# Performance work log

Hardware: AMD Instinct MI355X
Metric: run time of the kernel (lower is better)

The kernel has to match this reference:

```python
import jax, jax.numpy as jnp
import numpy as np

B, H, W = 1, 64, 64
Q = 256 * 256
CIN, ENC, HID, HEADS = 3, 64, 256, 16
HC = HID // HEADS
IN0 = (2 + HID) * 4 + 2   # 1034
IN1 = 2 + HID + 2         # 260


def conv3x3(x, w, b):
    y = jax.lax.conv_general_dilated(x, w, (1, 1), ((1, 1), (1, 1)),
                                     dimension_numbers=("NCHW", "OIHW", "NCHW"))
    return y + b[None, :, None, None]


def gelu(x):
    return jax.nn.gelu(x, approximate=False)


def mlp(x, w1, b1, w2, b2):
    # dropout p=0.0 -> identity
    return gelu(x @ w1 + b1) @ w2 + b2


def custom_ln(x, w, b, eps=1e-5):
    # torch .std() uses Bessel correction (ddof=1); note (std + eps), not var
    mean = x.mean(-1, keepdims=True)
    std = jnp.std(x, axis=-1, ddof=1, keepdims=True)
    return w * ((x - mean) / (std + eps)) + b


def qkv_attn(x, qkv_w, qkv_b, kln_w, kln_b, vln_w, vln_b, proj_w, proj_b):
    Bn, HWn, C = x.shape
    bias = x
    qkv = (x @ qkv_w + qkv_b).reshape(Bn, HWn, HEADS, 3 * HC).transpose(0, 2, 1, 3)
    q, k, v = jnp.split(qkv, 3, axis=-1)          # each [B, heads, HW, hc]
    k = custom_ln(k, kln_w, kln_b)
    v = custom_ln(v, vln_w, vln_b)
    kv = jnp.einsum("bhnc,bhnd->bhcd", k, v) / HWn  # linear attention: O(HW)
    v = jnp.einsum("bhnc,bhcd->bhnd", q, kv)
    v = v.transpose(0, 2, 1, 3).reshape(Bn, HWn, C)
    ret = v + bias
    return gelu(ret @ proj_w + proj_b) + bias


def _unnorm(c, size):  # align_corners=False
    return ((c + 1.0) * size - 1.0) / 2.0


def gs_nearest(img, coord_yx):
    # img [B,C,H,W]; coord_yx [B,Q,2] in (-1,1), (y,x) order (torch grid is flipped)
    Bn, C, Hn, Wn = img.shape
    iy = jnp.clip(jnp.round(_unnorm(coord_yx[..., 0], Hn)).astype(jnp.int32), 0, Hn - 1)
    ix = jnp.clip(jnp.round(_unnorm(coord_yx[..., 1], Wn)).astype(jnp.int32), 0, Wn - 1)
    flat = img.reshape(Bn, C, Hn * Wn)
    out = jnp.take_along_axis(flat, (iy * Wn + ix)[:, None, :], axis=2)  # [B,C,Q]
    return out.transpose(0, 2, 1)


def gs_bilinear(img, coord_yx, border=False):
    Bn, C, Hn, Wn = img.shape
    fy = _unnorm(coord_yx[..., 0], Hn)
    fx = _unnorm(coord_yx[..., 1], Wn)
    if border:
        fy = jnp.clip(fy, 0.0, Hn - 1.0)
        fx = jnp.clip(fx, 0.0, Wn - 1.0)
    y0 = jnp.floor(fy)
    x0 = jnp.floor(fx)
    wy = (fy - y0)[:, None, :]
    wx = (fx - x0)[:, None, :]
    y0i = y0.astype(jnp.int32)
    x0i = x0.astype(jnp.int32)
    flat = img.reshape(Bn, C, Hn * Wn)

    def gather(yi, xi):
        ok = (yi >= 0) & (yi < Hn) & (xi >= 0) & (xi < Wn)
        yc = jnp.clip(yi, 0, Hn - 1)
        xc = jnp.clip(xi, 0, Wn - 1)
        g = jnp.take_along_axis(flat, (yc * Wn + xc)[:, None, :], axis=2)
        return g * ok[:, None, :].astype(img.dtype)

    v00 = gather(y0i, x0i)
    v01 = gather(y0i, x0i + 1)
    v10 = gather(y0i + 1, x0i)
    v11 = gather(y0i + 1, x0i + 1)
    out = (v00 * (1 - wy) * (1 - wx) + v01 * (1 - wy) * wx +
           v10 * wy * (1 - wx) + v11 * wy * wx)
    return out.transpose(0, 2, 1)


def _forward(inp, coord, cell,
             enc_w, enc_b, freq_w, freq_b,
             out0_w1, out0_b1, out0_w2, out0_b2,
             out1_w1, out1_b1, out1_w2, out1_b2,
             a0_qkv_w, a0_qkv_b, a0_kln_w, a0_kln_b, a0_vln_w, a0_vln_b, a0_proj_w, a0_proj_b,
             a1_qkv_w, a1_qkv_b, a1_kln_w, a1_kln_b, a1_vln_w, a1_vln_b, a1_proj_w, a1_proj_b,
             fc1_w1, fc1_b1, fc1_w2, fc1_b2,
             fc2_w1, fc2_b1, fc2_w2, fc2_b2):
    Bq, Qn = coord.shape[:2]
    feat = conv3x3(inp, enc_w, enc_b)        # encoder stub [B,ENC,H,W]
    freq = conv3x3(feat, freq_w, freq_b)     # [B,HID,H,W]
    Hn, Wn = feat.shape[-2], feat.shape[-1]
    # make_coord(H,W): pixel-centered coords in (-1,1); channel0=y, channel1=x
    ys = -1.0 + (2.0 * jnp.arange(Hn, dtype=jnp.float32) + 1.0) / Hn
    xs = -1.0 + (2.0 * jnp.arange(Wn, dtype=jnp.float32) + 1.0) / Wn
    fc = jnp.stack(jnp.meshgrid(ys, xs, indexing="ij"), axis=0)  # [2,H,W]
    feat_coord = jnp.broadcast_to(fc[None], (Bq, 2, Hn, Wn))
    rx, ry = 1.0 / Hn, 1.0 / Wn               # 2/H/2, 2/W/2
    eps = 1e-6
    offs = jnp.array([[vx * rx + eps, vy * ry + eps]
                      for vx in (-1, 1) for vy in (-1, 1)], jnp.float32)  # [4,2]
    coord_s = jnp.clip(coord[None] + offs[:, None, None, :], -1 + 1e-6, 1 - 1e-6)  # [4,B,Q,2]
    q_freq = jax.vmap(gs_nearest, in_axes=(None, 0))(freq, coord_s)        # [4,B,Q,HID]
    q_coord = jax.vmap(gs_nearest, in_axes=(None, 0))(feat_coord, coord_s)  # [4,B,Q,2]
    scale = jnp.array([Hn, Wn], jnp.float32)
    rel = (coord[None] - q_coord) * scale                                  # [4,B,Q,2]
    areas = jnp.abs(rel[..., 0] * rel[..., 1]) + 1e-9                      # [4,B,Q]
    tot = areas.sum(0)
    areas_sw = areas[::-1]  # swap(0,3), swap(1,2)
    preds = q_freq * (areas_sw / tot)[..., None]
    rel_cell = cell * scale
    grid0 = jnp.concatenate([
        jnp.moveaxis(rel, 0, 2).reshape(Bq, Qn, 8),
        jnp.moveaxis(preds, 0, 2).reshape(Bq, Qn, 4 * HID),
        rel_cell], axis=-1)                                                # [B,Q,1034]
    grid_pred = gs_bilinear(freq, coord)                                   # [B,Q,HID]
    grid1 = jnp.concatenate([coord, grid_pred, rel_cell], axis=-1)         # [B,Q,260]
    x0 = qkv_attn(mlp(grid0, out0_w1, out0_b1, out0_w2, out0_b2),
                  a0_qkv_w, a0_qkv_b, a0_kln_w, a0_kln_b, a0_vln_w, a0_vln_b, a0_proj_w, a0_proj_b)
    x1 = qkv_attn(mlp(grid1, out1_w1, out1_b1, out1_w2, out1_b2),
                  a1_qkv_w, a1_qkv_b, a1_kln_w, a1_kln_b, a1_vln_w, a1_vln_b, a1_proj_w, a1_proj_b)
    f = x0 + x1
    result = mlp(f + gelu(mlp(f, fc1_w1, fc1_b1, fc1_w2, fc1_b2)),
                 fc2_w1, fc2_b1, fc2_w2, fc2_b2)                           # [B,Q,3]
    result_bil = gs_bilinear(inp, coord, border=True)                      # [B,Q,3]
    return result + result_bil


def setup_inputs() -> dict:
    key = jax.random.key(0)
    ks = iter(jax.random.split(key, 64))

    def n(shape, s=0.02):
        return jax.random.normal(next(ks), shape, jnp.float32) * s

    inp = jax.random.normal(next(ks), (B, CIN, H, W), jnp.float32)
    coord = jax.random.uniform(next(ks), (B, Q, 2), jnp.float32, -1.0, 1.0)
    cell = jnp.full((B, Q, 2), 2.0 / 256.0, jnp.float32)
    d = dict(inp=inp, coord=coord, cell=cell,
             enc_w=n((ENC, CIN, 3, 3)), enc_b=jnp.zeros((ENC,), jnp.float32),
             freq_w=n((HID, ENC, 3, 3)), freq_b=jnp.zeros((HID,), jnp.float32),
             out0_w1=n((IN0, HID)), out0_b1=jnp.zeros((HID,), jnp.float32),
             out0_w2=n((HID, HID)), out0_b2=jnp.zeros((HID,), jnp.float32),
             out1_w1=n((IN1, HID)), out1_b1=jnp.zeros((HID,), jnp.float32),
             out1_w2=n((HID, HID)), out1_b2=jnp.zeros((HID,), jnp.float32),
             fc1_w1=n((HID, HID)), fc1_b1=jnp.zeros((HID,), jnp.float32),
             fc1_w2=n((HID, HID)), fc1_b2=jnp.zeros((HID,), jnp.float32),
             fc2_w1=n((HID, HID)), fc2_b1=jnp.zeros((HID,), jnp.float32),
             fc2_w2=n((HID, 3)), fc2_b2=jnp.zeros((3,), jnp.float32))
    for p in ("a0", "a1"):
        d[p + "_qkv_w"] = n((HID, 3 * HID))
        d[p + "_qkv_b"] = jnp.zeros((3 * HID,), jnp.float32)
        d[p + "_kln_w"] = jnp.ones((HEADS, 1, HC), jnp.float32)
        d[p + "_kln_b"] = jnp.zeros((HEADS, 1, HC), jnp.float32)
        d[p + "_vln_w"] = jnp.ones((HEADS, 1, HC), jnp.float32)
        d[p + "_vln_b"] = jnp.zeros((HEADS, 1, HC), jnp.float32)
        d[p + "_proj_w"] = n((HID, HID))
        d[p + "_proj_b"] = jnp.zeros((HID,), jnp.float32)
    return d


def reference(inp, coord, cell,
              enc_w, enc_b, freq_w, freq_b,
              out0_w1, out0_b1, out0_w2, out0_b2,
              out1_w1, out1_b1, out1_w2, out1_b2,
              a0_qkv_w, a0_qkv_b, a0_kln_w, a0_kln_b, a0_vln_w, a0_vln_b, a0_proj_w, a0_proj_b,
              a1_qkv_w, a1_qkv_b, a1_kln_w, a1_kln_b, a1_vln_w, a1_vln_b, a1_proj_w, a1_proj_b,
              fc1_w1, fc1_b1, fc1_w2, fc1_b2,
              fc2_w1, fc2_b1, fc2_w2, fc2_b2):
    return _forward(inp, coord, cell,
                    enc_w, enc_b, freq_w, freq_b,
                    out0_w1, out0_b1, out0_w2, out0_b2,
                    out1_w1, out1_b1, out1_w2, out1_b2,
                    a0_qkv_w, a0_qkv_b, a0_kln_w, a0_kln_b, a0_vln_w, a0_vln_b, a0_proj_w, a0_proj_b,
                    a1_qkv_w, a1_qkv_b, a1_kln_w, a1_kln_b, a1_vln_w, a1_vln_b, a1_proj_w, a1_proj_b,
                    fc1_w1, fc1_b1, fc1_w2, fc1_b2,
                    fc2_w1, fc2_b1, fc2_w2, fc2_b2)
```

## Files before the change

### kernel.cpp

```cpp
#include <hip/hip_runtime.h>
#include <hip/hip_bf16.h>

#define DI __device__ __forceinline__

DI float gelu_f(float x){ return 0.5f*x*(1.0f + erff(x*0.7071067811865476f)); }
DI float bf2f(__hip_bfloat16 b){ return __bfloat162float(b); }
DI __hip_bfloat16 f2bf(float f){ return __float2bfloat16(f); }
DI float bflo(unsigned u){ return __uint_as_float(u<<16); }
DI float bfhi(unsigned u){ return __uint_as_float(u & 0xffff0000u); }
DI unsigned pack2bf(float a, float b){
  __hip_bfloat16 ha = f2bf(a), hb = f2bf(b);
  unsigned short ua = *reinterpret_cast<unsigned short*>(&ha);
  unsigned short ub = *reinterpret_cast<unsigned short*>(&hb);
  return (unsigned)ua | ((unsigned)ub<<16);
}

typedef __attribute__((ext_vector_type(8))) short bf16x8;
typedef __attribute__((ext_vector_type(4))) float f32x4;

template<typename T>
DI void load_lds16(const T* g, T* l){
  __builtin_amdgcn_global_load_lds((const __attribute__((address_space(1))) void*)g,
                                   (__attribute__((address_space(3))) void*)l, 16, 0, 0);
}
// ... 40 lines not shown
  int j = blockIdx.x, kk = threadIdx.x;
  float v;
  if(j < 1024){
    int s = j>>8, n = j&255;
    v = w0[(8 + 256*s + kk)*256 + n];
  } else {
    v = w1[(2 + kk)*256 + (j-1024)];
  }
  wt[(size_t)j*256 + kk] = f2bf(v);
}

struct PrepDesc { const float* src; __hip_bfloat16* dst; int mode; int pad; };
struct PrepArgs { PrepDesc d[13]; };
__global__ __launch_bounds__(256) void k_prep(PrepArgs a){
  int u = blockIdx.x >> 8, b = blockIdx.x & 255, t = threadIdx.x;
  PrepDesc d = a.d[u];
  float v;
  if(d.mode == 0) v = d.src[t*256 + b];
  else { int col = 48*(b>>4) + (d.mode-1) + (b&15); v = d.src[t*768 + col]; }
  d.dst[b*256 + t] = f2bf(v);
}

__global__ __launch_bounds__(256) void k_biasperm(const float* __restrict__ b0, const float* __restrict__ b1,
    const float* kw0, const float* kb0, const float* vw0, const float* vb0,
    const float* kw1, const float* kb1, const float* vw1, const float* vb1,
    float* __restrict__ dstB, float* __restrict__ lnw2, float* __restrict__ lnb2,
    __hip_bfloat16* __restrict__ zpage){
  int t = threadIdx.x;
  zpage[t] = f2bf(0.0f);
  #pragma unroll
  for(int br=0;br<2;br++){
    const float* s = br ? b1 : b0;
    #pragma unroll
    for(int part=0;part<3;part++)
      dstB[br*768 + part*256 + t] = s[48*(t>>4) + part*16 + (t&15)];
  }
  #pragma unroll
  for(int br=0;br<2;br++){
    #pragma unroll
    for(int half=0;half<2;half++){
      int j = half*256 + t;
      int h = j>>5, idx = j&31;
      bool isK = idx<16;
      int c = isK ? idx : idx-16;
      const float* w = isK ? (br?kw1:kw0) : (br?vw1:vw0);
      const float* bb= isK ? (br?kb1:kb0) : (br?vb1:vb0);
      lnw2[br*512 + j] = w[h*16+c];
      lnb2[br*512 + j] = bb[h*16+c];
    }
  }
}

template<int ADDI>
__global__ __launch_bounds__(256) void k_smallmm(const __hip_bfloat16* __restrict__ A,
    const __hip_bfloat16* __restrict__ B, __hip_bfloat16* __restrict__ C){
  __shared__ float ar[256];
  int i = blockIdx.x, t = threadIdx.x;
  float a = bf2f(A[(size_t)i*256 + t]);
  if(ADDI && t==i) a += 1.0f;
  ar[t] = a;
  __syncthreads();
  float a0=0.f,a1=0.f,a2=0.f,a3=0.f;
  for(int l=0;l<256;l+=4){
    a0 += ar[l+0]*bf2f(B[(l+0)*256 + t]);
    a1 += ar[l+1]*bf2f(B[(l+1)*256 + t]);
    a2 += ar[l+2]*bf2f(B[(l+2)*256 + t]);
    a3 += ar[l+3]*bf2f(B[(l+3)*256 + t]);
  }
  C[(size_t)i*256 + t] = f2bf((a0+a1)+(a2+a3));
}

__global__ __launch_bounds__(256) void k_smallmmR(const __hip_bfloat16* __restrict__ A,
    const __hip_bfloat16* __restrict__ B, __hip_bfloat16* __restrict__ C){
  __shared__ float ar[256];
  int j = blockIdx.x, t = threadIdx.x;
  int src = kvmap(j);
  ar[t] = bf2f(A[(size_t)src*256 + t]);
  __syncthreads();
  float a0=0.f,a1=0.f,a2=0.f,a3=0.f;
  for(int l=0;l<256;l+=4){
    a0 += ar[l+0]*bf2f(B[(l+0)*256 + t]);
    a1 += ar[l+1]*bf2f(B[(l+1)*256 + t]);
    a2 += ar[l+2]*bf2f(B[(l+2)*256 + t]);
    a3 += ar[l+3]*bf2f(B[(l+3)*256 + t]);
  }
  C[(size_t)j*256 + t] = f2bf((a0+a1)+(a2+a3));
}

__global__ __launch_bounds__(256) void k_bkv2R(const float* __restrict__ b2, const float* __restrict__ biaskv,
    const __hip_bfloat16* __restrict__ kvT_, float* __restrict__ outb){
  __shared__ float s_b2[256];
  int t = threadIdx.x; int n = blockIdx.x*256 + t;
  int src = kvmap(n);
  s_b2[t] = b2[t];
  __syncthreads();
  float v = biaskv[src];
  for(int l=0;l<256;l++) v += s_b2[l]*bf2f(kvT_[(size_t)src*256 + l]);
  outb[n] = v;
}

__global__ __launch_bounds__(256) void k_cvec(const float* __restrict__ b2, const float* __restrict__ bfold,
    const __hip_bfloat16* __restrict__ WfoldT, const __hip_bfloat16* __restrict__ projT_,
    const float* __restrict__ bp, float* __restrict__ c1){
  __shared__ float s_b2[256], s_r[256];
  int t = threadIdx.x;
  s_b2[t] = b2[t];
  __syncthreads();
  float r = s_b2[t] + bfold[t];
  for(int l=0;l<256;l++) r += s_b2[l]*bf2f(WfoldT[(size_t)t*256 + l]);
  s_r[t] = r;
  __syncthreads();
  float c = bp[t];
  for(int l=0;l<256;l++) c += s_r[l]*bf2f(projT_[(size_t)t*256 + l]);
  c1[t] = c;
}

__global__ __launch_bounds__(256) void k_sample(const float* __restrict__ coord, const float* __restrict__ inp,
    float* __restrict__ mf, int* __restrict__ mi, float* __restrict__ bil){
  int q = blockIdx.x*256 + threadIdx.x;
  float cy = coord[2*q], cx = coord[2*q+1];
  const float LO = (float)(-1.0 + 1e-6), HI = (float)(1.0 - 1e-6);
  const float ONEG = (float)(-1.0/64.0 + 1e-6), OPOS = (float)(1.0/64.0 + 1e-6);
  float areas[4];
  #pragma unroll
  for(int s=0;s<4;s++){
    float oy = (s<2)?ONEG:OPOS;
    float ox = (s&1)?OPOS:ONEG;
    float csy = fminf(fmaxf(cy+oy, LO), HI);
    float csx = fminf(fmaxf(cx+ox, LO), HI);
    float fy = ((csy+1.0f)*64.0f - 1.0f)*0.5f;
    float fx = ((csx+1.0f)*64.0f - 1.0f)*0.5f;
    int iy = (int)rintf(fy); iy = iy<0?0:(iy>63?63:iy);
    int ix = (int)rintf(fx); ix = ix<0?0:(ix>63?63:ix);
    float qcy = -1.0f + (float)(2*iy+1)*0.015625f;
    float qcx = -1.0f + (float)(2*ix+1)*0.015625f;
    float ry = (cy-qcy)*64.0f, rx = (cx-qcx)*64.0f;
    mf[q*16 + 4 + 2*s] = ry; mf[q*16 + 5 + 2*s] = rx;
    areas[s] = fabsf(ry*rx) + 1e-9f;
    mi[q*8 + s] = iy*64 + ix;
  }
  float tot = areas[0]+areas[1]+areas[2]+areas[3];
  #pragma unroll
  for(int s=0;s<4;s++) mf[q*16 + s] = areas[3-s] / tot;

  float fy = ((cy+1.0f)*64.0f - 1.0f)*0.5f;
  float fx = ((cx+1.0f)*64.0f - 1.0f)*0.5f;
  {
    float y0 = floorf(fy), x0 = floorf(fx);
    float wy = fy-y0, wx = fx-x0;
    int y0i = (int)y0, x0i = (int)x0;
    float cw[4] = {(1.0f-wy)*(1.0f-wx), (1.0f-wy)*wx, wy*(1.0f-wx), wy*wx};
    #pragma unroll
    for(int c2=0;c2<4;c2++){
      int yi = y0i + (c2>>1), xi = x0i + (c2&1);
      bool ok = (yi>=0 && yi<64 && xi>=0 && xi<64);
      int yc = yi<0?0:(yi>63?63:yi), xc = xi<0?0:(xi>63?63:xi);
      mf[q*16 + 12 + c2] = ok ? cw[c2] : 0.0f;
      mi[q*8 + 4 + c2] = yc*64 + xc;
    }
  }
  {
    float fyb = fminf(fmaxf(fy, 0.0f), 63.0f);
    float fxb = fminf(fmaxf(fx, 0.0f), 63.0f);
    float y0 = floorf(fyb), x0 = floorf(fxb);
    float wy = fyb-y0, wx = fxb-x0;
    int y0i = (int)y0, x0i = (int)x0;
    float cw[4] = {(1.0f-wy)*(1.0f-wx), (1.0f-wy)*wx, wy*(1.0f-wx), wy*wx};
    float a0=0,a1=0,a2=0;
    #pragma unroll
    for(int c2=0;c2<4;c2++){
      int yi = y0i + (c2>>1), xi = x0i + (c2&1);
      if(yi>=0 && yi<64 && xi>=0 && xi<64){
        int idx = yi*64+xi; float wgt = cw[c2];
        a0 += inp[idx]*wgt; a1 += inp[4096+idx]*wgt; a2 += inp[8192+idx]*wgt;
      }
    }
    bil[q*3+0]=a0; bil[q*3+1]=a1; bil[q*3+2]=a2;
  }
}

template<int BR>
__global__ __launch_bounds__(256) void k_stage1(const __hip_bfloat16* __restrict__ P, const float* __restrict__ mf,
    const int* __restrict__ mi, const float* __restrict__ coord, const float* __restrict__ cell,
    const float* __restrict__ W1, const float* __restrict__ b1, __hip_bfloat16* __restrict__ out){
  __shared__ float wsm[11][256];
  int j = threadIdx.x;
  if(BR==0){
    #pragma unroll
    for(int r=0;r<8;r++) wsm[r][j] = W1[r*256 + j];
    wsm[8][j] = W1[1032*256 + j];
    wsm[9][j] = W1[1033*256 + j];
    wsm[10][j] = b1[j];
  } else {
    wsm[0][j] = W1[0*256 + j];
    wsm[1][j] = W1[1*256 + j];
    wsm[2][j] = W1[258*256 + j];
    wsm[3][j] = W1[259*256 + j];
    wsm[4][j] = b1[j];
  }
  __syncthreads();
  int q0 = blockIdx.x*32;
  for(int qq=0;qq<32;qq++){
    int q = q0+qq;
    float acc;
    const float* m = mf + q*16;
    const int* ii = mi + q*8;
    if(BR==0){
      acc = wsm[10][j];
      #pragma unroll
      for(int r=0;r<8;r++) acc += m[4+r]*wsm[r][j];
      float cly = cell[2*q]*64.0f, clx = cell[2*q+1]*64.0f;
      acc += cly*wsm[8][j] + clx*wsm[9][j];
      #pragma unroll
      for(int s=0;s<4;s++) acc += m[s]*bf2f(P[(size_t)ii[s]*1280 + s*256 + j]);
    } else {
      acc = wsm[4][j];
      float cy = coord[2*q], cx = coord[2*q+1];
      float cly = cell[2*q]*64.0f, clx = cell[2*q+1]*64.0f;
      acc += cy*wsm[0][j] + cx*wsm[1][j] + cly*wsm[2][j] + clx*wsm[3][j];
      #pragma unroll
      for(int c2=0;c2<4;c2++) acc += m[12+c2]*bf2f(P[(size_t)ii[4+c2]*1280 + 1024 + j]);
    }
    out[(size_t)q*256 + j] = f2bf(gelu_f(acc));
  }
}

template<int ACT,int NRES>
__global__ __launch_bounds__(512) void k_gemm_mfma(
    const __hip_bfloat16* __restrict__ A, const __hip_bfloat16* __restrict__ BT,
    const float* __restrict__ bias, const __hip_bfloat16* __restrict__ R1,
    const __hip_bfloat16* __restrict__ R2, __hip_bfloat16* __restrict__ C,
    int M, int N, int K, int ldc){
  __shared__ __align__(1024) char smem[64*133*4];
  const int t = threadIdx.x, wave = t>>6, lane = t&63;
  const int MT = M>>7, NT = N>>7;
  const int b = blockIdx.x, xcd = b&7, i = b>>3;
  const int nt = i % NT, mtl = i / NT;
  const int m0 = (xcd*(MT>>3) + mtl) << 7, n0 = nt << 7;
  const int wr = (wave>>2)*64, wc = (wave&3)*32;
  const int lr = lane&15, lh = lane>>4;

  f32x4 acc[4][2] = {};
  const int ntiles = K>>6;
  for(int kt=0; kt<ntiles; ++kt){
    __syncthreads();
    #pragma unroll
    for(int q2=0;q2<2;q2++){
      int c = (wave*2+q2)*64 + lane;
      int row = c>>3; int k8 = (c&7) ^ (row&7);
      __hip_bfloat16* la = (__hip_bfloat16*)smem + (size_t)(wave*2+q2)*512;
      __hip_bfloat16* lb = (__hip_bfloat16*)(smem + 16384) + (size_t)(wave*2+q2)*512;
      load_lds16(A  + (size_t)(m0+row)*K + (kt*64 + k8*8), la);
      load_lds16(BT + (size_t)(n0+row)*K + (kt*64 + k8*8), lb);
    }
    __syncthreads();
    const __hip_bfloat16* Ab = (const __hip_bfloat16*)smem;
    const __hip_bfloat16* Bb = (const __hip_bfloat16*)(smem + 16384);
    #pragma unroll
    for(int kk=0;kk<2;kk++){
      bf16x8 af[4], bfr[2];
// ... 113 lines not shown
        int p = (kk*4 + lh) ^ (row&7);
        af[m] = *reinterpret_cast<const bf16x8*>(Ab + row*64 + p*8);
      }
      #pragma unroll
      for(int n=0;n<4;n++){
        int row = wc + n*16 + lr;
        int p = (kk*4 + lh) ^ (row&7);
        bfr[n] = *reinterpret_cast<const bf16x8*>(Bb + row*64 + p*8);
      }
      #pragma unroll
      for(int m=0;m<4;m++)
        #pragma unroll
        for(int n=0;n<4;n++)
          acc[m][n] = __builtin_amdgcn_mfma_f32_16x16x32_bf16(af[m], bfr[n], acc[m][n], 0,0,0);
    }
  }

  float* epi = (float*)smem;
  const int cg = t&3;
  #pragma unroll
  for(int hf=0; hf<2; ++hf){
    __syncthreads();
    if((wave>>1) == hf){
      #pragma unroll
      for(int m=0;m<4;m++)
        #pragma unroll
        for(int n=0;n<4;n++){
          int col = wc + n*16 + lr;
          #pragma unroll
          for(int j=0;j<4;j++)
            epi[(m*16 + lh*4 + j)*133 + col] = acc[m][n][j];
        }
    }
    __syncthreads();
    const int lrow = t>>2, c0 = cg*32;
    const size_t grow = (size_t)(m0 + hf*64 + lrow);
    const float* er = epi + lrow*133;
    #pragma unroll
    for(int g0=0; g0<4; g0++){
      int g = (g0 + cg) & 3;
      int cb = c0 + g*8;
      int gc = n0 + cb;
      float v[8];
      #pragma unroll
      for(int e=0;e<8;e++) v[e] = er[cb+e] + bias[gc+e];
      uint4 o;
      o.x = pack2bf(v[0],v[1]); o.y = pack2bf(v[2],v[3]);
      o.z = pack2bf(v[4],v[5]); o.w = pack2bf(v[6],v[7]);
      *reinterpret_cast<uint4*>(C + grow*256 + gc) = o;
    }
  }
}

__global__ __launch_bounds__(512) void k_kvln(
    const __hip_bfloat16* __restrict__ A, const __hip_bfloat16* __restrict__ BT,
    const float* __restrict__ bias, const float* __restrict__ lnw, const float* __restrict__ lnb,
    float* __restrict__ kvpart){
  __shared__ __align__(1024) char smem[34816];
  const int t = threadIdx.x, wave = t>>6, lane = t&63;
  const int MT = 512, NT = 4;
  const int b = blockIdx.x, xcd = b&7, i = b>>3;
  const int nt = i % NT, mtl = i / NT;
  const int m0 = (xcd*(MT>>3) + mtl) << 7, n0 = nt << 7;
  const int wr = (wave>>2)*64, wc = (wave&3)*32;
  const int lr = lane&15, lh = lane>>4;

  f32x4 acc[4][2] = {};
  for(int kt=0; kt<4; ++kt){
    __syncthreads();
    #pragma unroll
    for(int q2=0;q2<2;q2++){
      int c = (wave*2+q2)*64 + lane;
      int row = c>>3; int k8 = (c&7) ^ (row&7);
      __hip_bfloat16* la = (__hip_bfloat16*)smem + (size_t)(wave*2+q2)*512;
      __hip_bfloat16* lb = (__hip_bfloat16*)(smem + 16384) + (size_t)(wave*2+q2)*512;
      load_lds16(A  + (size_t)(m0+row)*256 + (kt*64 + k8*8), la);
      load_lds16(BT + (size_t)(n0+row)*256 + (kt*64 + k8*8), lb);
    }
    __syncthreads();
    const __hip_bfloat16* Ab = (const __hip_bfloat16*)smem;
    const __hip_bfloat16* Bb = (const __hip_bfloat16*)(smem + 16384);
    #pragma unroll
    for(int kk=0;kk<2;kk++){
      bf16x8 af[4], bfr[2];
      #pragma unroll
      for(int m=0;m<4;m++){
        int row = wr + m*16 + lr;
        int p = (kk*4 + lh) ^ (row&7);
        af[m] = *reinterpret_cast<const bf16x8*>(Ab + row*64 + p*8);
      }
      #pragma unroll
      for(int n=0;n<2;n++){
        int row = wc + n*16 + lr;
        int p = (kk*4 + lh) ^ (row&7);
        bfr[n] = *reinterpret_cast<const bf16x8*>(Bb + row*64 + p*8);
      }
      #pragma unroll
      for(int m=0;m<4;m++)
        #pragma unroll
        for(int n=0;n<2;n++)
          acc[m][n] = __builtin_amdgcn_mfma_f32_16x16x32_bf16(af[m], bfr[n], acc[m][n], 0,0,0);
    }
  }
  __syncthreads();

  __hip_bfloat16* knT = (__hip_bfloat16*)smem;
  __hip_bfloat16* vnT = (__hip_bfloat16*)(smem + 17408);
  #pragma unroll
  for(int m=0;m<4;m++){
    #pragma unroll
    for(int n=0;n<2;n++){
      int cl = wc + n*16 + lr;
      int gcol = n0 + cl;
      float bs = bias[gcol];
      int h2 = cl>>5, isV = (cl>>4)&1;
      short4 pk;
      #pragma unroll
      for(int j=0;j<4;j++) ((__hip_bfloat16*)&pk)[j] = f2bf(acc[m][n][j] + bs);
      int r = wr + m*16 + lh*4;
      __hip_bfloat16* dst = (isV ? vnT : knT) + (h2*16 + lr)*136 + r;
      *reinterpret_cast<short4*>(dst) = pk;
    }
  }
  __syncthreads();
  #pragma unroll
  for(int i4=0; i4<2; ++i4){
    int task = i4*512 + t;
    int r = task & 127, hv = task >> 7;
    int h2 = hv >> 1, isV = hv & 1;
    __hip_bfloat16* base = (isV ? vnT : knT) + (h2*16)*136 + r;
    float xs[16];
    float s=0.0f, s2=0.0f;
    #pragma unroll
    for(int c=0;c<16;c++){ xs[c] = bf2f(base[c*136]); s += xs[c]; s2 += xs[c]*xs[c]; }
    float mean = s*0.0625f;
    float var = (s2 - 16.0f*mean*mean)*(1.0f/15.0f); var = var<0.0f?0.0f:var;
    float inv = 1.0f/(sqrtf(var) + 1e-5f);
    int gbase = n0 + h2*32 + isV*16;
    #pragma unroll
    for(int c=0;c<16;c++)
      base[c*136] = f2bf(lnw[gbase+c]*((xs[c]-mean)*inv) + lnb[gbase+c]);
  }
  __syncthreads();
  {
    const int hloc = wave>>1, kh = wave&1;
    f32x4 kacc = {};
    #pragma unroll
    for(int kk=0;kk<2;kk++){
      int off = kh*64 + kk*32 + lh*8;
      bf16x8 af  = *reinterpret_cast<const bf16x8*>(knT + (hloc*16 + lr)*136 + off);
      bf16x8 bf_ = *reinterpret_cast<const bf16x8*>(vnT + (hloc*16 + lr)*136 + off);
      kacc = __builtin_amdgcn_mfma_f32_16x16x32_bf16(af, bf_, kacc, 0,0,0);
    }
    const int mt = m0>>7;
    const int hglob = nt*4 + hloc;
    #pragma unroll
    for(int j=0;j<4;j++)
      kvpart[((size_t)mt*2 + kh)*4096 + hglob*256 + (lh*4+j)*16 + lr] = kacc[j];
  }
}

template<int NRES>
__global__ __launch_bounds__(512) void k_gemm12(
    const __hip_bfloat16* __restrict__ A, const __hip_bfloat16* __restrict__ B1T,
    const float* __restrict__ c1, const __hip_bfloat16* __restrict__ B2T,
    const float* __restrict__ b2, const __hip_bfloat16* __restrict__ R,
    __hip_bfloat16* __restrict__ C){
  __shared__ __align__(1024) char smem[49152];
  const int t = threadIdx.x, wave = t>>6, lane = t&63;
  const int MT = 512, NT = 2;
  const int b = blockIdx.x, xcd = b&7, i = b>>3;
  const int nt = i % NT, mtl = i / NT;
  const int m0 = (xcd*(MT>>3) + mtl) << 7, n0 = nt << 7;
  const int wr = (wave>>2)*64, wc = (wave&3)*32;
  const int lr = lane&15, lh = lane>>4;
  f32x4 acc1[4][2] = {}, acc2[4][2] = {};
  for(int k0=0;k0<256;k0+=64){
    __syncthreads();
    #pragma unroll
    for(int q2=0;q2<2;q2++){
      int c = (wave*2+q2)*64 + lane;
      int row = c>>3; int k8 = (c&7) ^ (row&7);
      __hip_bfloat16* base = (__hip_bfloat16*)smem + (size_t)(wave*2+q2)*512;
      load_lds16(A   + (size_t)(m0+row)*256 + (k0 + k8*8), base);
      load_lds16(B1T + (size_t)(n0+row)*256 + (k0 + k8*8), base + 8192);
      load_lds16(B2T + (size_t)(n0+row)*256 + (k0 + k8*8), base + 16384);
    }
    __syncthreads();
    const __hip_bfloat16* Ab = (const __hip_bfloat16*)smem;
    #pragma unroll
    for(int kk=0;kk<2;kk++){
      bf16x8 af[4], bfr[2];
      #pragma unroll
      for(int m=0;m<4;m++){
        int row = wr + m*16 + lr;
        int p = (kk*4 + lh) ^ (row&7);
        af[m] = *reinterpret_cast<const bf16x8*>(Ab + row*64 + p*8);
      }
      #pragma unroll
      for(int n=0;n<2;n++){
        int row = wc + n*16 + lr;
        int p = (kk*4 + lh) ^ (row&7);
        bfr[n] = *reinterpret_cast<const bf16x8*>(Ab + 8192 + row*64 + p*8);
      }
      #pragma unroll
      for(int m=0;m<4;m++)
        #pragma unroll
        for(int n=0;n<2;n++)
          acc1[m][n] = __builtin_amdgcn_mfma_f32_16x16x32_bf16(af[m], bfr[n], acc1[m][n], 0,0,0);
      #pragma unroll
      for(int n=0;n<2;n++){
// ... 118 lines not shown
      for(int m=0;m<4;m++)
        #pragma unroll
        for(int n=0;n<2;n++)
          acc[m][n] = __builtin_amdgcn_mfma_f32_16x16x32_bf16(af[m], bfr[n], acc[m][n], 0,0,0);
    }
  }

  float* epi = (float*)smem;
  #pragma unroll
  for(int hf=0; hf<2; ++hf){
    __syncthreads();
    if((wave>>2) == hf){
      #pragma unroll
      for(int m=0;m<4;m++)
        #pragma unroll
        for(int n=0;n<2;n++){
          int col = wc + n*16 + lr;
          #pragma unroll
          for(int j=0;j<4;j++)
            epi[(m*16 + lh*4 + j)*133 + col] = acc[m][n][j];
        }
    }
    __syncthreads();
    {
      const int lrow = t>>3, c0 = (t&7)*16;
      const float* er = epi + lrow*133;
      float s0=0.f, s1=0.f, s2=0.f;
      #pragma unroll
      for(int e=0;e<16;e++){
        int gc = n0 + c0 + e;
        float v = gelu_f(er[c0+e] + bias[gc]);
        s0 += v*w4s[gc*3+0];
        s1 += v*w4s[gc*3+1];
        s2 += v*w4s[gc*3+2];
      }
      s0 += __shfl_xor(s0,1); s0 += __shfl_xor(s0,2); s0 += __shfl_xor(s0,4);
      s1 += __shfl_xor(s1,1); s1 += __shfl_xor(s1,2); s1 += __shfl_xor(s1,4);
      s2 += __shfl_xor(s2,1); s2 += __shfl_xor(s2,2); s2 += __shfl_xor(s2,4);
      if((t&7)==0){
        float* pp = part + (size_t)nt*196608 + (size_t)(m0 + hf*64 + lrow)*3;
        pp[0]=s0; pp[1]=s1; pp[2]=s2;
      }
    }
  }
}

__global__ __launch_bounds__(256) void k_combine(const float* __restrict__ part, const float* __restrict__ b4,
    const float* __restrict__ bil, float* __restrict__ out){
  int i = blockIdx.x*256 + threadIdx.x;
  int j = i - (i/3)*3;
  out[i] = part[i] + part[196608 + i] + b4[j] + bil[i];
}

__global__ __launch_bounds__(256) void k_kvred(const float* __restrict__ kvpart, float* __restrict__ kv){
  __shared__ float sm[256];
  int b = blockIdx.x, t = threadIdx.x;
  int d = t & 15, seg = t >> 4;
  float s = 0.0f;
  for(int k=0;k<64;k++) s += kvpart[(size_t)(seg*64+k)*4096 + b*16 + d];
  sm[t] = s;
  __syncthreads();
  if(t < 16){
    float r = 0.0f;
    #pragma unroll
    for(int g=0; g<16; g++) r += sm[g*16 + t];
    kv[b*16 + t] = r * (1.0f/65536.0f);
  }
}

__global__ __launch_bounds__(256) void k_fold(const __hip_bfloat16* __restrict__ qT,
    const float* __restrict__ biasq, const float* __restrict__ kv,
    __hip_bfloat16* __restrict__ WfoldT, float* __restrict__ bfold){
  int n = blockIdx.x, t = threadIdx.x;
  int h = n>>4, d = n&15;
  float s = 0.0f;
  #pragma unroll
  for(int c=0;c<16;c++)
    s += bf2f(qT[(size_t)(h*16+c)*256 + t]) * kv[h*256 + c*16 + d];
  WfoldT[(size_t)n*256 + t] = f2bf(s);
  if(t==0){
    float b=0.0f;
    #pragma unroll
    for(int c=0;c<16;c++) b += biasq[h*16+c]*kv[h*256+c*16+d];
    bfold[n]=b;
  }
}

extern "C" void kernel_launch(void* const* d_in, const int* in_sizes, int n_in,
                              void* d_out, int out_size, void* d_ws, size_t ws_size,
                              hipStream_t stream){
  (void)in_sizes; (void)n_in; (void)out_size;
  const float* inp     = (const float*)d_in[0];
  const float* coord   = (const float*)d_in[1];
  const float* cell    = (const float*)d_in[2];
  const float* enc_w   = (const float*)d_in[3];
  const float* enc_b   = (const float*)d_in[4];
  const float* freq_w  = (const float*)d_in[5];
  const float* freq_b  = (const float*)d_in[6];
  const float* out0_w1 = (const float*)d_in[7];
  const float* out0_b1 = (const float*)d_in[8];
  const float* out0_w2 = (const float*)d_in[9];
  const float* out0_b2 = (const float*)d_in[10];
  const float* out1_w1 = (const float*)d_in[11];
  const float* out1_b1 = (const float*)d_in[12];
  const float* out1_w2 = (const float*)d_in[13];
  const float* out1_b2 = (const float*)d_in[14];
  const float* fc1_w1  = (const float*)d_in[15];
  const float* fc1_b1  = (const float*)d_in[16];
  const float* fc1_w2  = (const float*)d_in[17];
  const float* fc1_b2  = (const float*)d_in[18];
  const float* fc2_w1  = (const float*)d_in[19];
  const float* fc2_b1  = (const float*)d_in[20];
  const float* fc2_w2  = (const float*)d_in[21];
  const float* fc2_b2  = (const float*)d_in[22];
  const float* qkv_w[2] = {(const float*)d_in[23], (const float*)d_in[31]};
  const float* qkv_b[2] = {(const float*)d_in[24], (const float*)d_in[32]};
  const float* kln_w[2] = {(const float*)d_in[25], (const float*)d_in[33]};
  const float* kln_b[2] = {(const float*)d_in[26], (const float*)d_in[34]};
  const float* vln_w[2] = {(const float*)d_in[27], (const float*)d_in[35]};
  const float* vln_b[2] = {(const float*)d_in[28], (const float*)d_in[36]};
  const float* proj_w[2] = {(const float*)d_in[29], (const float*)d_in[37]};
  const float* proj_b[2] = {(const float*)d_in[30], (const float*)d_in[38]};
  const float* b2arr[2] = {out0_b2, out1_b2};

  char* wsp = (char*)d_ws; size_t off = 0;
  auto alloc = [&](size_t bytes)->void*{ void* p = wsp + off; off += (bytes + 255) & ~(size_t)255; return p; };
  __hip_bfloat16* featP = (__hip_bfloat16*)alloc(262144ull*2);
  __hip_bfloat16* zpage = (__hip_bfloat16*)alloc(256ull*2);
  __hip_bfloat16* wtb = (__hip_bfloat16*)alloc(2097152ull*2);
  __hip_bfloat16* P = (__hip_bfloat16*)alloc(5242880ull*2);
  float* mf     = (float*)alloc(65536ull*16*4);
  int*   mi     = (int*)alloc(65536ull*8*4);
  float* bil    = (float*)alloc(65536ull*3*4);
  float* kvpart = (float*)alloc(1024ull*4096*4);
  float* kv0    = (float*)alloc(4096ull*4);
  float* kv1    = (float*)alloc(4096ull*4);
  float* biasbuf= (float*)alloc(1536ull*4);
  float* lnbuf  = (float*)alloc(2048ull*4);
  float* bfold  = (float*)alloc(256ull*4);
  float* c1     = (float*)alloc(256ull*4);
  float* bkvh   = (float*)alloc(1024ull*4);
  float* part   = (float*)alloc(2ull*196608*4);
  __hip_bfloat16* wfoldT = (__hip_bfloat16*)alloc(65536ull*2);
  __hip_bfloat16* bufA = (__hip_bfloat16*)alloc(65536ull*256*2);
  __hip_bfloat16* bufB = (__hip_bfloat16*)alloc(65536ull*256*2);
  __hip_bfloat16* bufC = (__hip_bfloat16*)alloc(65536ull*256*2);
  if(off > ws_size) return;

  __hip_bfloat16* w2T[2]   = {wtb,          wtb + 65536};
  __hip_bfloat16* projT[2] = {wtb + 131072, wtb + 196608};
  __hip_bfloat16* fc1w1T   =  wtb + 262144;
  __hip_bfloat16* fc1w2T   =  wtb + 327680;
  __hip_bfloat16* fc2w1T   =  wtb + 393216;
  __hip_bfloat16* qT[2]    = {wtb + 458752, wtb + 655360};
  __hip_bfloat16* kvT[2]   = {wtb + 524288, wtb + 720896};
  __hip_bfloat16* wfreqT   =  wtb + 851968;
  __hip_bfloat16* wblkT    =  wtb + 1015808;
  __hip_bfloat16* kvh2T[2] = {wtb + 1343488, wtb + 1474560};
  __hip_bfloat16* Ubuf     =  wtb + 1605632;
  __hip_bfloat16* M1T      =  wtb + 1671168;
  __hip_bfloat16* freqB = bufB;

  k_conv1<<<1024,256,0,stream>>>(inp, enc_w, enc_b, featP);
  k_wfreq<<<256,256,0,stream>>>(freq_w, wfreqT);
  k_wblk<<<1280,256,0,stream>>>(out0_w1, out1_w1, wblkT);

  PrepArgs pa;
  pa.d[0]  = {out0_w2,   w2T[0],   0, 0};
  pa.d[1]  = {out1_w2,   w2T[1],   0, 0};
  pa.d[2]  = {proj_w[0], projT[0], 0, 0};
  pa.d[3]  = {proj_w[1], projT[1], 0, 0};
  pa.d[4]  = {fc1_w1,    fc1w1T,   0, 0};
  pa.d[5]  = {fc1_w2,    fc1w2T,   0, 0};
  pa.d[6]  = {fc2_w1,    fc2w1T,   0, 0};
  pa.d[7]  = {qkv_w[0],  qT[0],    1, 0};
  pa.d[8]  = {qkv_w[0],  kvT[0],   17, 0};
  pa.d[9]  = {qkv_w[0],  kvT[0]+65536, 33, 0};
  pa.d[10] = {qkv_w[1],  qT[1],    1, 0};
  pa.d[11] = {qkv_w[1],  kvT[1],   17, 0};
  pa.d[12] = {qkv_w[1],  kvT[1]+65536, 33, 0};
  k_prep<<<13*256,256,0,stream>>>(pa);
  k_biasperm<<<1,256,0,stream>>>(qkv_b[0], qkv_b[1],
      kln_w[0], kln_b[0], vln_w[0], vln_b[0], kln_w[1], kln_b[1], vln_w[1], vln_b[1],
      biasbuf, lnbuf, lnbuf + 1024, zpage);

  for(int br=0;br<2;br++){
    k_smallmmR<<<512,256,0,stream>>>(kvT[br], w2T[br], kvh2T[br]);
    k_bkv2R<<<2,256,0,stream>>>(b2arr[br], biasbuf + br*768 + 256, kvT[br], bkvh + br*512);
  }

  k_gfreq<<<64,256,0,stream>>>(featP, zpage, wfreqT, freq_b, freqB);
  k_gemm_mfma<0,0><<<320,512,0,stream>>>(freqB, wblkT, nullptr, nullptr,nullptr, P, 4096,1280,256, 1280);

  k_sample<<<256,256,0,stream>>>(coord, inp, mf, mi, bil);

  for(int br=0;br<2;br++){
    if(br==0) k_stage1<0><<<2048,256,0,stream>>>(P, mf, mi, coord, cell, out0_w1, out0_b1, bufA);
    else      k_stage1<1><<<2048,256,0,stream>>>(P, mf, mi, coord, cell, out1_w1, out1_b1, bufA);
    k_kvln<<<2048,512,0,stream>>>(bufA, kvh2T[br], bkvh + br*512, lnbuf + br*512, lnbuf + 1024 + br*512, kvpart);
    float* kvf = br ? kv1 : kv0;
    k_kvred<<<256,256,0,stream>>>(kvpart, kvf);
    k_fold<<<256,256,0,stream>>>(qT[br], biasbuf + br*768, kvf, wfoldT, bfold);
    k_smallmm<1><<<256,256,0,stream>>>(wfoldT, w2T[br], Ubuf);
    k_smallmm<0><<<256,256,0,stream>>>(projT[br], Ubuf, M1T);
    k_cvec<<<1,256,0,stream>>>(b2arr[br], bfold, wfoldT, projT[br], proj_b[br], c1);
    if(br==0)
      k_gemm12<0><<<1024,512,0,stream>>>(bufA, M1T, c1, w2T[0], b2arr[0], nullptr, bufC);
    else
      k_gemm12<1><<<1024,512,0,stream>>>(bufA, M1T, c1, w2T[1], b2arr[1], bufC, bufC);
  }
  k_gemm_mfma<1,0><<<1024,512,0,stream>>>(bufC, fc1w1T, fc1_b1, nullptr,nullptr, bufA, 65536,256,256, 256);
  k_gemm_mfma<1,1><<<1024,512,0,stream>>>(bufA, fc1w2T, fc1_b2, bufC, nullptr, bufB, 65536,256,256, 256);
  k_gemmF<<<1024,512,0,stream>>>(bufB, fc2w1T, fc2_b1, fc2_w2, part);
  k_combine<<<768,256,0,stream>>>(part, fc2_b2, bil, (float*)d_out);
}
```

Before: 467.9 us.

## Batch both attention branches into single launches per stage

Each per-branch kernel (small matmuls, bias, stage1, kv layernorm, reduction, fold, cvec) now handles both branches in one launch, with the branch picked from the block index. Separate buffers are kept for each branch. This removes about a dozen kernel launches and puts the small kernels' blocks into one grid, which fills the GPU better. In exchange it needs an extra 32MB activation buffer and a doubled kvpart scratch, which adds memory footprint and some cache pressure.

```diff
diff --git a/kernel.cpp b/kernel.cpp
--- a/kernel.cpp
+++ b/kernel.cpp
@@ -116,10 +116,15 @@
 }
 
 template<int ADDI>
-__global__ __launch_bounds__(256) void k_smallmm(const __hip_bfloat16* __restrict__ A,
-    const __hip_bfloat16* __restrict__ B, __hip_bfloat16* __restrict__ C){
+__global__ __launch_bounds__(256) void k_smallmm2(
+    const __hip_bfloat16* __restrict__ A0, const __hip_bfloat16* __restrict__ A1,
+    const __hip_bfloat16* __restrict__ B0, const __hip_bfloat16* __restrict__ B1,
+    __hip_bfloat16* __restrict__ C0, __hip_bfloat16* __restrict__ C1){
   __shared__ float ar[256];
-  int i = blockIdx.x, t = threadIdx.x;
+  int br = blockIdx.x >> 8, i = blockIdx.x & 255, t = threadIdx.x;
+  const __hip_bfloat16* A = br ? A1 : A0;
+  const __hip_bfloat16* B = br ? B1 : B0;
+  __hip_bfloat16* C = br ? C1 : C0;
   float a = bf2f(A[(size_t)i*256 + t]);
   if(ADDI && t==i) a += 1.0f;
   ar[t] = a;
@@ -134,10 +139,15 @@
   C[(size_t)i*256 + t] = f2bf((a0+a1)+(a2+a3));
 }
 
-__global__ __launch_bounds__(256) void k_smallmmR(const __hip_bfloat16* __restrict__ A,
-    const __hip_bfloat16* __restrict__ B, __hip_bfloat16* __restrict__ C){
+__global__ __launch_bounds__(256) void k_smallmmR2(
+    const __hip_bfloat16* __restrict__ A0, const __hip_bfloat16* __restrict__ A1,
+    const __hip_bfloat16* __restrict__ B0, const __hip_bfloat16* __restrict__ B1,
+    __hip_bfloat16* __restrict__ C0, __hip_bfloat16* __restrict__ C1){
   __shared__ float ar[256];
-  int j = blockIdx.x, t = threadIdx.x;
+  int br = blockIdx.x >> 9, j = blockIdx.x & 511, t = threadIdx.x;
+  const __hip_bfloat16* A = br ? A1 : A0;
+  const __hip_bfloat16* B = br ? B1 : B0;
+  __hip_bfloat16* C = br ? C1 : C0;
   int src = kvmap(j);
   ar[t] = bf2f(A[(size_t)src*256 + t]);
   __syncthreads();
@@ -151,32 +161,43 @@
   C[(size_t)j*256 + t] = f2bf((a0+a1)+(a2+a3));
 }
 
-__global__ __launch_bounds__(256) void k_bkv2R(const float* __restrict__ b2, const float* __restrict__ biaskv,
-    const __hip_bfloat16* __restrict__ kvT_, float* __restrict__ outb){
+__global__ __launch_bounds__(256) void k_bkv2R2(const float* __restrict__ b20, const float* __restrict__ b21,
+    const float* __restrict__ biaskv,
+    const __hip_bfloat16* __restrict__ kvT0, const __hip_bfloat16* __restrict__ kvT1,
+    float* __restrict__ outb){
   __shared__ float s_b2[256];
-  int t = threadIdx.x; int n = blockIdx.x*256 + t;
+  int br = blockIdx.x >> 1, nb = blockIdx.x & 1, t = threadIdx.x;
+  int n = nb*256 + t;
+  const float* b2 = br ? b21 : b20;
+  const __hip_bfloat16* kvT_ = br ? kvT1 : kvT0;
   int src = kvmap(n);
   s_b2[t] = b2[t];
   __syncthreads();
-  float v = biaskv[src];
+  float v = biaskv[br*768 + 256 + src];
   for(int l=0;l<256;l++) v += s_b2[l]*bf2f(kvT_[(size_t)src*256 + l]);
-  outb[n] = v;
-}
-
-__global__ __launch_bounds__(256) void k_cvec(const float* __restrict__ b2, const float* __restrict__ bfold,
-    const __hip_bfloat16* __restrict__ WfoldT, const __hip_bfloat16* __restrict__ projT_,
-    const float* __restrict__ bp, float* __restrict__ c1){
+  outb[br*512 + n] = v;
+}
+
+__global__ __launch_bounds__(256) void k_cvec2(const float* __restrict__ b20, const float* __restrict__ b21,
+    const float* __restrict__ bfold,
+    const __hip_bfloat16* __restrict__ WfoldT,
+    const __hip_bfloat16* __restrict__ projT0, const __hip_bfloat16* __restrict__ projT1,
+    const float* __restrict__ bp0, const float* __restrict__ bp1, float* __restrict__ c1){
   __shared__ float s_b2[256], s_r[256];
-  int t = threadIdx.x;
+  int br = blockIdx.x, t = threadIdx.x;
+  const float* b2 = br ? b21 : b20;
+  const __hip_bfloat16* Wf = WfoldT + (size_t)br*65536;
+  const __hip_bfloat16* pj = br ? projT1 : projT0;
+  const float* bp = br ? bp1 : bp0;
   s_b2[t] = b2[t];
   __syncthreads();
-  float r = s_b2[t] + bfold[t];
-  for(int l=0;l<256;l++) r += s_b2[l]*bf2f(WfoldT[(size_t)t*256 + l]);
+  float r = s_b2[t] + bfold[br*256 + t];
+  for(int l=0;l<256;l++) r += s_b2[l]*bf2f(Wf[(size_t)t*256 + l]);
   s_r[t] = r;
   __syncthreads();
   float c = bp[t];
-  for(int l=0;l<256;l++) c += s_r[l]*bf2f(projT_[(size_t)t*256 + l]);
-  c1[t] = c;
+  for(int l=0;l<256;l++) c += s_r[l]*bf2f(pj[(size_t)t*256 + l]);
+  c1[br*256 + t] = c;
 }
 
 __global__ __launch_bounds__(256) void k_sample(const float* __restrict__ coord, const float* __restrict__ inp,
@@ -243,33 +264,37 @@
   }
 }
 
-template<int BR>
-__global__ __launch_bounds__(256) void k_stage1(const __hip_bfloat16* __restrict__ P, const float* __restrict__ mf,
+__global__ __launch_bounds__(256) void k_stage1both(const __hip_bfloat16* __restrict__ P, const float* __restrict__ mf,
     const int* __restrict__ mi, const float* __restrict__ coord, const float* __restrict__ cell,
-    const float* __restrict__ W1, const float* __restrict__ b1, __hip_bfloat16* __restrict__ out){
+    const float* __restrict__ W1_0, const float* __restrict__ b1_0,
+    const float* __restrict__ W1_1, const float* __restrict__ b1_1,
+    __hip_bfloat16* __restrict__ outA0, __hip_bfloat16* __restrict__ outA1){
   __shared__ float wsm[11][256];
+  const int br = blockIdx.x >> 11;
+  const int blk = blockIdx.x & 2047;
   int j = threadIdx.x;
-  if(BR==0){
-    #pragma unroll
-    for(int r=0;r<8;r++) wsm[r][j] = W1[r*256 + j];
-    wsm[8][j] = W1[1032*256 + j];
-    wsm[9][j] = W1[1033*256 + j];
-    wsm[10][j] = b1[j];
+  if(br==0){
+    #pragma unroll
+    for(int r=0;r<8;r++) wsm[r][j] = W1_0[r*256 + j];
+    wsm[8][j] = W1_0[1032*256 + j];
+    wsm[9][j] = W1_0[1033*256 + j];
+    wsm[10][j] = b1_0[j];
   } else {
-    wsm[0][j] = W1[0*256 + j];
-    wsm[1][j] = W1[1*256 + j];
-    wsm[2][j] = W1[258*256 + j];
-    wsm[3][j] = W1[259*256 + j];
-    wsm[4][j] = b1[j];
-  }
+    wsm[0][j] = W1_1[0*256 + j];
+    wsm[1][j] = W1_1[1*256 + j];
+    wsm[2][j] = W1_1[258*256 + j];
+    wsm[3][j] = W1_1[259*256 + j];
+    wsm[4][j] = b1_1[j];
+  }
+  __hip_bfloat16* out = br ? outA1 : outA0;
   __syncthreads();
-  int q0 = blockIdx.x*32;
+  int q0 = blk*32;
   for(int qq=0;qq<32;qq++){
     int q = q0+qq;
     float acc;
     const float* m = mf + q*16;
     const int* ii = mi + q*8;
-    if(BR==0){
+    if(br==0){
       acc = wsm[10][j];
       #pragma unroll
       for(int r=0;r<8;r++) acc += m[4+r]*wsm[r][j];
@@ -489,18 +514,25 @@
   }
 }
 
-__global__ __launch_bounds__(512) void k_kvln(
-    const __hip_bfloat16* __restrict__ A, const __hip_bfloat16* __restrict__ BT,
-    const float* __restrict__ bias, const float* __restrict__ lnw, const float* __restrict__ lnb,
+__global__ __launch_bounds__(512) void k_kvlnboth(
+    const __hip_bfloat16* __restrict__ A0, const __hip_bfloat16* __restrict__ A1,
+    const __hip_bfloat16* __restrict__ BT0, const __hip_bfloat16* __restrict__ BT1,
+    const float* __restrict__ biasAll, const float* __restrict__ lnwAll, const float* __restrict__ lnbAll,
     float* __restrict__ kvpart){
   __shared__ __align__(1024) char smem[34816];
   const int t = threadIdx.x, wave = t>>6, lane = t&63;
   const int MT = 512, NT = 4;
-  const int b = blockIdx.x, xcd = b&7, i = b>>3;
+  const int br = blockIdx.x >> 11;
+  const int b = blockIdx.x & 2047, xcd = b&7, i = b>>3;
   const int nt = i % NT, mtl = i / NT;
   const int m0 = (xcd*(MT>>3) + mtl) << 7, n0 = nt << 7;
   const int wr = (wave>>2)*64, wc = (wave&3)*32;
   const int lr = lane&15, lh = lane>>4;
+  const __hip_bfloat16* A = br ? A1 : A0;
+  const __hip_bfloat16* BT = br ? BT1 : BT0;
+  const float* bias = biasAll + br*512;
+  const float* lnw = lnwAll + br*512;
+  const float* lnb = lnbAll + br*512;
 
   f32x4 acc[4][2] = {};
   for(int kt=0; kt<4; ++kt){
@@ -593,7 +625,7 @@
     const int hglob = nt*4 + hloc;
     #pragma unroll
     for(int j=0;j<4;j++)
-      kvpart[((size_t)mt*2 + kh)*4096 + hglob*256 + (lh*4+j)*16 + lr] = kacc[j];
+      kvpart[((size_t)br*1024 + (size_t)mt*2 + kh)*4096 + hglob*256 + (lh*4+j)*16 + lr] = kacc[j];
   }
 }
 
@@ -818,38 +850,67 @@
   out[i] = part[i] + part[196608 + i] + b4[j] + bil[i];
 }
 
-__global__ __launch_bounds__(256) void k_kvred(const float* __restrict__ kvpart, float* __restrict__ kv){
+__global__ __launch_bounds__(256) void k_kvredboth(const float* __restrict__ kvpart,
+    float* __restrict__ kv0, float* __restrict__ kv1){
   __shared__ float sm[256];
-  int b = blockIdx.x, t = threadIdx.x;
+  int br = blockIdx.x >> 8, b = blockIdx.x & 255, t = threadIdx.x;
   int d = t & 15, seg = t >> 4;
+  const float* src = kvpart + (size_t)br*1024*4096;
   float s = 0.0f;
-  for(int k=0;k<64;k++) s += kvpart[(size_t)(seg*64+k)*4096 + b*16 + d];
+  for(int k=0;k<64;k++) s += src[(size_t)(seg*64+k)*4096 + b*16 + d];
   sm[t] = s;
   __syncthreads();
   if(t < 16){
     float r = 0.0f;
     #pragma unroll
     for(int g=0; g<16; g++) r += sm[g*16 + t];
-    kv[b*16 + t] = r * (1.0f/65536.0f);
-  }
-}
-
-__global__ __launch_bounds__(256) void k_fold(const __hip_bfloat16* __restrict__ qT,
-    const float* __restrict__ biasq, const float* __restrict__ kv,
+    (br ? kv1 : kv0)[b*16 + t] = r * (1.0f/65536.0f);
+  }
+}
+
+__global__ __launch_bounds__(256) void k_foldboth(
+    const __hip_bfloat16* __restrict__ qT0, const __hip_bfloat16* __restrict__ qT1,
+    const float* __restrict__ biasqAll, const float* __restrict__ kv0, const float* __restrict__ kv1,
     __hip_bfloat16* __restrict__ WfoldT, float* __restrict__ bfold){
-  int n = blockIdx.x, t = threadIdx.x;
+  int br = blockIdx.x >> 8, n = blockIdx.x & 255, t = threadIdx.x;
+  const __hip_bfloat16* qT = br ? qT1 : qT0;
+  const float* biasq = biasqAll + br*768;
+  const float* kv = br ? kv1 : kv0;
   int h = n>>4, d = n&15;
   float s = 0.0f;
   #pragma unroll
   for(int c=0;c<16;c++)
     s += bf2f(qT[(size_t)(h*16+c)*256 + t]) * kv[h*256 + c*16 + d];
-  WfoldT[(size_t)n*256 + t] = f2bf(s);
+  WfoldT[(size_t)br*65536 + (size_t)n*256 + t] = f2bf(s);
   if(t==0){
     float b=0.0f;
     #pragma unroll
     for(int c=0;c<16;c++) b += biasq[h*16+c]*kv[h*256+c*16+d];
-    bfold[n]=b;
-  }
+    bfold[br*256 + n]=b;
+  }
+}
+
+__global__ __launch_bounds__(256) void k_smallmmI2(
+    const __hip_bfloat16* __restrict__ WfoldT,
+    const __hip_bfloat16* __restrict__ B0, const __hip_bfloat16* __restrict__ B1,
+    __hip_bfloat16* __restrict__ C0, __hip_bfloat16* __restrict__ C1){
+  __shared__ float ar[256];
+  int br = blockIdx.x >> 8, i = blockIdx.x & 255, t = threadIdx.x;
+  const __hip_bfloat16* A = WfoldT + (size_t)br*65536;
+  const __hip_bfloat16* B = br ? B1 : B0;
+  __hip_bfloat16* C = br ? C1 : C0;
+  float a = bf2f(A[(size_t)i*256 + t]);
+  if(t==i) a += 1.0f;
+  ar[t] = a;
+  __syncthreads();
+  float a0=0.f,a1=0.f,a2=0.f,a3=0.f;
+  for(int l=0;l<256;l+=4){
+    a0 += ar[l+0]*bf2f(B[(l+0)*256 + t]);
+    a1 += ar[l+1]*bf2f(B[(l+1)*256 + t]);
+    a2 += ar[l+2]*bf2f(B[(l+2)*256 + t]);
+    a3 += ar[l+3]*bf2f(B[(l+3)*256 + t]);
+  }
+  C[(size_t)i*256 + t] = f2bf((a0+a1)+(a2+a3));
 }
 
 extern "C" void kernel_launch(void* const* d_in, const int* in_sizes, int n_in,
@@ -887,7 +948,6 @@
   const float* vln_b[2] = {(const float*)d_in[28], (const float*)d_in[36]};
   const float* proj_w[2] = {(const float*)d_in[29], (const float*)d_in[37]};
   const float* proj_b[2] = {(const float*)d_in[30], (const float*)d_in[38]};
-  const float* b2arr[2] = {out0_b2, out1_b2};
 
   char* wsp = (char*)d_ws; size_t off = 0;
   auto alloc = [&](size_t bytes)->void*{ void* p = wsp + off; off += (bytes + 255) & ~(size_t)255; return p; };
@@ -898,17 +958,18 @@
   float* mf     = (float*)alloc(65536ull*16*4);
   int*   mi     = (int*)alloc(65536ull*8*4);
   float* bil    = (float*)alloc(65536ull*3*4);
-  float* kvpart = (float*)alloc(1024ull*4096*4);
+  float* kvpart = (float*)alloc(2048ull*4096*4);
   float* kv0    = (float*)alloc(4096ull*4);
   float* kv1    = (float*)alloc(4096ull*4);
   float* biasbuf= (float*)alloc(1536ull*4);
   float* lnbuf  = (float*)alloc(2048ull*4);
-  float* bfold  = (float*)alloc(256ull*4);
-  float* c1     = (float*)alloc(256ull*4);
+  float* bfold  = (float*)alloc(512ull*4);
+  float* c1     = (float*)alloc(512ull*4);
   float* bkvh   = (float*)alloc(1024ull*4);
   float* part   = (float*)alloc(2ull*196608*4);
-  __hip_bfloat16* wfoldT = (__hip_bfloat16*)alloc(65536ull*2);
-  __hip_bfloat16* bufA = (__hip_bfloat16*)alloc(65536ull*256*2);
+  __hip_bfloat16* wfoldT = (__hip_bfloat16*)alloc(131072ull*2);
+  __hip_bfloat16* bufA0 = (__hip_bfloat16*)alloc(65536ull*256*2);
+  __hip_bfloat16* bufA1 = (__hip_bfloat16*)alloc(65536ull*256*2);
   __hip_bfloat16* bufB = (__hip_bfloat16*)alloc(65536ull*256*2);
   __hip_bfloat16* bufC = (__hip_bfloat16*)alloc(65536ull*256*2);
   if(off > ws_size) return;
@@ -923,8 +984,8 @@
   __hip_bfloat16* wfreqT   =  wtb + 851968;
   __hip_bfloat16* wblkT    =  wtb + 1015808;
   __hip_bfloat16* kvh2T[2] = {wtb + 1343488, wtb + 1474560};
-  __hip_bfloat16* Ubuf     =  wtb + 1605632;
-  __hip_bfloat16* M1T      =  wtb + 1671168;
+  __hip_bfloat16* Ubuf[2]  = {wtb + 1605632, wtb + 1671168};
+  __hip_bfloat16* M1T[2]   = {wtb + 1736704, wtb + 1802240};
   __hip_bfloat16* freqB = bufB;
 
   k_conv1<<<1024,256,0,stream>>>(inp, enc_w, enc_b, featP);
@@ -950,33 +1011,27 @@
       kln_w[0], kln_b[0], vln_w[0], vln_b[0], kln_w[1], kln_b[1], vln_w[1], vln_b[1],
       biasbuf, lnbuf, lnbuf + 1024, zpage);
 
-  for(int br=0;br<2;br++){
-    k_smallmmR<<<512,256,0,stream>>>(kvT[br], w2T[br], kvh2T[br]);
-    k_bkv2R<<<2,256,0,stream>>>(b2arr[br], biasbuf + br*768 + 256, kvT[br], bkvh + br*512);
-  }
+  k_smallmmR2<<<1024,256,0,stream>>>(kvT[0], kvT[1], w2T[0], w2T[1], kvh2T[0], kvh2T[1]);
+  k_bkv2R2<<<4,256,0,stream>>>(out0_b2, out1_b2, biasbuf, kvT[0], kvT[1], bkvh);
 
   k_gfreq<<<64,256,0,stream>>>(featP, zpage, wfreqT, freq_b, freqB);
   k_gemm_mfma<0,0><<<320,512,0,stream>>>(freqB, wblkT, nullptr, nullptr,nullptr, P, 4096,1280,256, 1280);
 
   k_sample<<<256,256,0,stream>>>(coord, inp, mf, mi, bil);
 
-  for(int br=0;br<2;br++){
-    if(br==0) k_stage1<0><<<2048,256,0,stream>>>(P, mf, mi, coord, cell, out0_w1, out0_b1, bufA);
-    else      k_stage1<1><<<2048,256,0,stream>>>(P, mf, mi, coord, cell, out1_w1, out1_b1, bufA);
-    k_kvln<<<2048,512,0,stream>>>(bufA, kvh2T[br], bkvh + br*512, lnbuf + br*512, lnbuf + 1024 + br*512, kvpart);
-    float* kvf = br ? kv1 : kv0;
-    k_kvred<<<256,256,0,stream>>>(kvpart, kvf);
-    k_fold<<<256,256,0,stream>>>(qT[br], biasbuf + br*768, kvf, wfoldT, bfold);
-    k_smallmm<1><<<256,256,0,stream>>>(wfoldT, w2T[br], Ubuf);
-    k_smallmm<0><<<256,256,0,stream>>>(projT[br], Ubuf, M1T);
-    k_cvec<<<1,256,0,stream>>>(b2arr[br], bfold, wfoldT, projT[br], proj_b[br], c1);
-    if(br==0)
-      k_gemm12<0><<<1024,512,0,stream>>>(bufA, M1T, c1, w2T[0], b2arr[0], nullptr, bufC);
-    else
-      k_gemm12<1><<<1024,512,0,stream>>>(bufA, M1T, c1, w2T[1], b2arr[1], bufC, bufC);
-  }
-  k_gemm_mfma<1,0><<<1024,512,0,stream>>>(bufC, fc1w1T, fc1_b1, nullptr,nullptr, bufA, 65536,256,256, 256);
-  k_gemm_mfma<1,1><<<1024,512,0,stream>>>(bufA, fc1w2T, fc1_b2, bufC, nullptr, bufB, 65536,256,256, 256);
+  k_stage1both<<<4096,256,0,stream>>>(P, mf, mi, coord, cell, out0_w1, out0_b1, out1_w1, out1_b1, bufA0, bufA1);
+  k_kvlnboth<<<4096,512,0,stream>>>(bufA0, bufA1, kvh2T[0], kvh2T[1], bkvh, lnbuf, lnbuf + 1024, kvpart);
+  k_kvredboth<<<512,256,0,stream>>>(kvpart, kv0, kv1);
+  k_foldboth<<<512,256,0,stream>>>(qT[0], qT[1], biasbuf, kv0, kv1, wfoldT, bfold);
+  k_smallmmI2<<<512,256,0,stream>>>(wfoldT, w2T[0], w2T[1], Ubuf[0], Ubuf[1]);
+  k_smallmm2<0><<<512,256,0,stream>>>(projT[0], projT[1], Ubuf[0], Ubuf[1], M1T[0], M1T[1]);
+  k_cvec2<<<2,256,0,stream>>>(out0_b2, out1_b2, bfold, wfoldT, projT[0], projT[1], proj_b[0], proj_b[1], c1);
+
+  k_gemm12<0><<<1024,512,0,stream>>>(bufA0, M1T[0], c1,       w2T[0], out0_b2, nullptr, bufC);
+  k_gemm12<1><<<1024,512,0,stream>>>(bufA1, M1T[1], c1 + 256, w2T[1], out1_b2, bufC, bufC);
+
+  k_gemm_mfma<1,0><<<1024,512,0,stream>>>(bufC, fc1w1T, fc1_b1, nullptr,nullptr, bufA0, 65536,256,256, 256);
+  k_gemm_mfma<1,1><<<1024,512,0,stream>>>(bufA0, fc1w2T, fc1_b2, bufC, nullptr, bufB, 65536,256,256, 256);
   k_gemmF<<<1024,512,0,stream>>>(bufB, fc2w1T, fc2_b1, fc2_w2, part);
   k_combine<<<768,256,0,stream>>>(part, fc2_b2, bil, (float*)d_out);
 }
```

Result: faster. 439.6 us (-6.0%).
